# Optimization experiments

Measured on AMD Instinct MI355X. Metric: run time of the kernel, lower is better.

The kernel has to match this reference:

```python
import jax, jax.numpy as jnp
import numpy as np
from jax import lax

NL = 2        # num mamba layers
D_MODEL = 200
D_STATE = 16
D_CONV = 4
DI = 400      # expand * d_model
DT_RANK = 13  # ceil(d_model / 16)
B = 256
L = 256
EPS = 1e-12


def _ln(x, w, b):
    mu = jnp.mean(x, axis=-1, keepdims=True)
    var = jnp.mean((x - mu) ** 2, axis=-1, keepdims=True)
    return (x - mu) / jnp.sqrt(var + EPS) * w + b


def _mamba(x, in_proj_w, conv_w, conv_b, x_proj_w, dt_proj_w, dt_proj_b, A_log, D, out_proj_w):
    b, l, _ = x.shape
    xz = jnp.einsum('bld,ed->ble', x, in_proj_w)  # [b,l,2*DI]
    xc, z = jnp.split(xz, 2, axis=-1)
    # causal depthwise conv over time (pad d_conv-1 on the left == pytorch pad+slice)
    xt = xc.transpose(0, 2, 1)  # [b,DI,l]
    xt = lax.conv_general_dilated(xt, conv_w[:, None, :], (1,), [(D_CONV - 1, 0)],
                                  dimension_numbers=('NCH', 'OIH', 'NCH'),
                                  feature_group_count=DI)
    xc = jax.nn.silu(xt + conv_b[None, :, None]).transpose(0, 2, 1)  # [b,l,DI]
    x_dbl = jnp.einsum('bld,ed->ble', xc, x_proj_w)  # [b,l,DT_RANK+2*N]
    dt = x_dbl[..., :DT_RANK]
    Bm = x_dbl[..., DT_RANK:DT_RANK + D_STATE]
    Cm = x_dbl[..., DT_RANK + D_STATE:]
    delta = jax.nn.softplus(jnp.einsum('blr,dr->bld', dt, dt_proj_w) + dt_proj_b)  # [b,l,DI]
    A = -jnp.exp(A_log)  # [DI,N]

    def step(h, inp):
        d_t, u_t, B_t, C_t = inp  # [b,DI],[b,DI],[b,N],[b,N]
        dA = jnp.exp(d_t[..., None] * A)  # [b,DI,N]
        h = dA * h + (d_t * u_t)[..., None] * B_t[:, None, :]
        y = jnp.einsum('bdn,bn->bd', h, C_t)
        return h, y

    h0 = jnp.zeros((b, DI, D_STATE), dtype=x.dtype)
    xs = (delta.transpose(1, 0, 2), xc.transpose(1, 0, 2),
          Bm.transpose(1, 0, 2), Cm.transpose(1, 0, 2))
    _, ys = lax.scan(step, h0, xs)
    y = ys.transpose(1, 0, 2) + xc * D  # [b,l,DI]
    y = y * jax.nn.silu(z)
    return jnp.einsum('bld,ed->ble', y, out_proj_w)


def _forward(item_emb, in_proj_w, conv_w, conv_b, x_proj_w, dt_proj_w, dt_proj_b,
             A_log, D, out_proj_w, ln1_w, ln1_b, ffn_w1, ffn_b1, ffn_w2, ffn_b2,
             ffn_ln_w, ffn_ln_b):
    h = item_emb
    for i in range(NL):
        m = _mamba(h, in_proj_w[i], conv_w[i], conv_b[i], x_proj_w[i],
                   dt_proj_w[i], dt_proj_b[i], A_log[i], D[i], out_proj_w[i])
        h = _ln(m + h, ln1_w[i], ln1_b[i])  # num_layers > 1 -> residual branch
        f = jnp.einsum('bld,ed->ble', h, ffn_w1[i]) + ffn_b1[i]
        f = jax.nn.gelu(f, approximate=False)  # torch nn.GELU default = exact
        f = jnp.einsum('ble,de->bld', f, ffn_w2[i]) + ffn_b2[i]
        h = _ln(f + h, ffn_ln_w[i], ffn_ln_b[i])
    c = h[:, -1:, :]
    x_n = h[:, :-1, :]
    return c, x_n


def setup_inputs() -> dict:
    key = jax.random.key(0)
    ks = jax.random.split(key, 10)
    s = 0.02
    f32 = jnp.float32
    A_log = jnp.broadcast_to(jnp.log(jnp.arange(1, D_STATE + 1, dtype=f32)),
                             (NL, DI, D_STATE))
    return {
        'item_emb': jax.random.normal(ks[0], (B, L, D_MODEL), f32),
        'item_seq_len': jax.random.randint(ks[1], (B,), 1, L, jnp.int32),
        'in_proj_w': s * jax.random.normal(ks[2], (NL, 2 * DI, D_MODEL), f32),
        'conv_w': s * jax.random.normal(ks[3], (NL, DI, D_CONV), f32),
        'conv_b': jnp.zeros((NL, DI), f32),
        'x_proj_w': s * jax.random.normal(ks[4], (NL, DT_RANK + 2 * D_STATE, DI), f32),
        'dt_proj_w': s * jax.random.normal(ks[5], (NL, DI, DT_RANK), f32),
        'dt_proj_b': s * jax.random.normal(ks[6], (NL, DI), f32),
        'A_log': A_log,
        'D': jnp.ones((NL, DI), f32),
        'out_proj_w': s * jax.random.normal(ks[7], (NL, D_MODEL, DI), f32),
        'ln1_w': jnp.ones((NL, D_MODEL), f32),
        'ln1_b': jnp.zeros((NL, D_MODEL), f32),
        'ffn_w1': s * jax.random.normal(ks[8], (NL, 4 * D_MODEL, D_MODEL), f32),
        'ffn_b1': jnp.zeros((NL, 4 * D_MODEL), f32),
        'ffn_w2': s * jax.random.normal(ks[9], (NL, D_MODEL, 4 * D_MODEL), f32),
        'ffn_b2': jnp.zeros((NL, D_MODEL), f32),
        'ffn_ln_w': jnp.ones((NL, D_MODEL), f32),
        'ffn_ln_b': jnp.zeros((NL, D_MODEL), f32),
    }


def reference(item_emb, item_seq_len, in_proj_w, conv_w, conv_b, x_proj_w,
              dt_proj_w, dt_proj_b, A_log, D, out_proj_w, ln1_w, ln1_b,
              ffn_w1, ffn_b1, ffn_w2, ffn_b2, ffn_ln_w, ffn_ln_b):
    # item_seq_len is accepted but unused by Mamba4Rec.forward
    return _forward(item_emb, in_proj_w, conv_w, conv_b, x_proj_w, dt_proj_w,
                    dt_proj_b, A_log, D, out_proj_w, ln1_w, ln1_b, ffn_w1,
                    ffn_b1, ffn_w2, ffn_b2, ffn_ln_w, ffn_ln_b)
```

## Files before the change

### kernel.cpp

```cpp
#include <hip/hip_runtime.h>
#include <hip/hip_bf16.h>

#define DM 200
#define DIE 400
#define LSEQ 256
#define NB 256

typedef __hip_bfloat16 bf16;
typedef const float* fp;
typedef __attribute__((ext_vector_type(8))) short short8;
typedef __attribute__((ext_vector_type(4))) short short4_t;
typedef __attribute__((ext_vector_type(4))) float f32x4;

__device__ __forceinline__ float b2f(bf16 x) { return __bfloat162float(x); }
__device__ __forceinline__ bf16  f2b(float x) { return __float2bfloat16(x); }

__device__ __forceinline__ unsigned short f2bbits(float f) {
    union { float f; unsigned int u; } c; c.f = f;
    unsigned int u = c.u;
    unsigned int r = (u + 0x7fffu + ((u >> 16) & 1u)) >> 16;
    return (unsigned short)r;
}
__device__ __forceinline__ void stf(float* p, float v) { *p = v; }
__device__ __forceinline__ void stf(bf16* p, float v) { *p = f2b(v); }

#define W_XP_OFF 320000
#define W_OP_OFF 356000
#define W_F1_OFF 516000
#define W_F2_OFF 836000
#define W_TOTAL  1156000
#define W_BYTES  2312000

__global__ __launch_bounds__(256) void wcvt_kernel(fp a0, fp a1, fp a2, fp a3, fp a4,
                                                   bf16* __restrict__ dst) {
    int g = blockIdx.x * 256 + threadIdx.x;
    if (g >= W_TOTAL / 4) return;
    int idx = g * 4;
    const float* src;
    int off;
    if (idx < W_XP_OFF)      { src = a0; off = idx; }
    else if (idx < W_OP_OFF) { src = a1; off = idx - W_XP_OFF; }
    else if (idx < W_F1_OFF) { src = a2; off = idx - W_OP_OFF; }
    else if (idx < W_F2_OFF) { src = a3; off = idx - W_F1_OFF; }
    else                     { src = a4; off = idx - W_F2_OFF; }
    float4 v = *(const float4*)(src + off);
    short4_t o;
    o.x = (short)f2bbits(v.x); o.y = (short)f2bbits(v.y);
    o.z = (short)f2bbits(v.z); o.w = (short)f2bbits(v.w);
    *(short4_t*)((short*)dst + idx) = o;
}

__global__ __launch_bounds__(256) void cvt_kernel(const float* __restrict__ src,
                                                  bf16* __restrict__ dst, int n4) {
    int g = blockIdx.x * 256 + threadIdx.x;
    if (g >= n4) return;
    int idx = g * 4;
    float4 v = *(const float4*)(src + idx);
    short4_t o;
    o.x = (short)f2bbits(v.x); o.y = (short)f2bbits(v.y);
    o.z = (short)f2bbits(v.z); o.w = (short)f2bbits(v.w);
    *(short4_t*)((short*)dst + idx) = o;
}

template <typename TC, int EPI>
__global__ __launch_bounds__(256) void gemm_mfma(const bf16* __restrict__ A, int lda,
                                                 const bf16* __restrict__ W,
                                                 const float* __restrict__ bias,
                                                 TC* __restrict__ C, int ldc,
                                                 int N, int K) {
    constexpr int LS = 40;
    __shared__ short As[128 * LS];
    __shared__ short Bs[128 * LS];
    const int m0 = blockIdx.x * 128;
    const int n0 = blockIdx.y * 128;
    const int tid = threadIdx.x;
    const int wave = tid >> 6;
    const int lane = tid & 63;
    const int wm = (wave & 1) * 64;
    const int wn = (wave >> 1) * 64;
    const int fm = lane & 15;
    const int quad = lane >> 4;

    f32x4 acc[4][4] = {};

    const int sr = tid >> 1;
    const int sc = (tid & 1) * 16;

    for (int k0 = 0; k0 < K; k0 += 32) {
        {
            const short* src = (const short*)A + (size_t)(m0 + sr) * lda + k0 + sc;
            short* dst = As + sr * LS + sc;
            if (k0 + sc + 16 <= K) {
                *(short8*)dst = *(const short8*)src;
                *(short8*)(dst + 8) = *(const short8*)(src + 8);
            } else {
#pragma unroll
                for (int j = 0; j < 16; ++j)
                    dst[j] = (k0 + sc + j < K) ? src[j] : (short)0;
            }
        }
        {
            short* dst = Bs + sr * LS + sc;
            if (n0 + sr < N) {
                const short* src = (const short*)W + (size_t)(n0 + sr) * K + k0 + sc;
                if (k0 + sc + 16 <= K) {
                    *(short8*)dst = *(const short8*)src;
                    *(short8*)(dst + 8) = *(const short8*)(src + 8);
                } else {
#pragma unroll
                    for (int j = 0; j < 16; ++j)
                        dst[j] = (k0 + sc + j < K) ? src[j] : (short)0;
                }
            } else {
#pragma unroll
                for (int j = 0; j < 16; ++j) dst[j] = 0;
            }
        }
        __syncthreads();
        short8 af[4], bfr[4];
#pragma unroll
        for (int i = 0; i < 4; ++i)
            af[i] = *(const short8*)(As + (wm + i * 16 + fm) * LS + quad * 8);
#pragma unroll
        for (int j = 0; j < 4; ++j)
            bfr[j] = *(const short8*)(Bs + (wn + j * 16 + fm) * LS + quad * 8);
#pragma unroll
        for (int i = 0; i < 4; ++i)
#pragma unroll
            for (int j = 0; j < 4; ++j)
                acc[i][j] = __builtin_amdgcn_mfma_f32_16x16x32_bf16(af[i], bfr[j], acc[i][j], 0, 0, 0);
        __syncthreads();
    }

#pragma unroll
    for (int j = 0; j < 4; ++j) {
        int n = n0 + wn + j * 16 + fm;
        if (n >= N) continue;
        float bv = (EPI == 2 || EPI == 3) ? bias[n] : 0.f;
#pragma unroll
        for (int i = 0; i < 4; ++i) {
#pragma unroll
            for (int r = 0; r < 4; ++r) {
                int m = m0 + wm + i * 16 + quad * 4 + r;
                float v = acc[i][j][r];
                if (EPI == 2) {
                    v += bv;
                    v = 0.5f * v * (1.f + erff(v * 0.70710678118654752f));
                } else if (EPI == 3) {
                    v += bv;
                } else if (EPI == 5) {
                    if (n >= 400) v = v * __builtin_amdgcn_rcpf(1.f + __expf(-v));
                }
                stf(&C[(size_t)m * ldc + n], v);
            }
        }
    }
}

__global__ __launch_bounds__(256) void conv_silu_inplace(bf16* __restrict__ xz,
                                                         const float* __restrict__ cw,
                                                         const float* __restrict__ cb,
                                                         int total ) {
    int idx = blockIdx.x * 256 + threadIdx.x;
    if (idx >= total) return;
    int d = idx % DIE;
    int b = idx / DIE;
    float w0 = cw[d * 4 + 0];
    float w1 = cw[d * 4 + 1];
    float w2 = cw[d * 4 + 2];
    float w3 = cw[d * 4 + 3];
    float bias = cb[d];
    float x0 = 0.f, x1 = 0.f, x2 = 0.f;
    bf16* p = xz + (size_t)b * LSEQ * 800 + d;
    for (int t = 0; t < LSEQ; ++t) {
        float x = b2f(*p);
        float s = bias + w0 * x0 + w1 * x1 + w2 * x2 + w3 * x;
        x0 = x1; x1 = x2; x2 = x;
        float sig = __builtin_amdgcn_rcpf(1.f + __expf(-s));
        *p = f2b(s * sig);
        p += 800;
    }
}

template <bool FAST>
__device__ __forceinline__ void scan_body(const float* __restrict__ rp,
                                          bf16* __restrict__ xp,
                                          const float* Wr, const float* A2,
                                          float bdt, float Dv) {
    float h[16];
#pragma unroll
    for (int n = 0; n < 16; ++n) h[n] = 0.f;

    auto precomp = [&](int o45, int ox,
                       float* Bb, float* Cb, float* dA, float& du, float& ut, float& zs) {
        float dtv = bdt;
#pragma unroll
        for (int r = 0; r < 13; ++r) dtv += Wr[r] * rp[o45 + r];
#pragma unroll
        for (int j = 0; j < 16; ++j) { Bb[j] = rp[o45 + 13 + j]; Cb[j] = rp[o45 + 29 + j]; }
        ut = b2f(xp[ox]);
        zs = b2f(xp[ox + 400]);
        float sp = (dtv > 20.f) ? dtv : __logf(1.f + __expf(dtv));
        if (FAST) {
            float r1 = __expf(-sp);
            float r2 = r1 * r1, r3 = r2 * r1, r4 = r2 * r2;
            float r5 = r4 * r1, r6 = r4 * r2, r7 = r4 * r3, r8 = r4 * r4;
            dA[0] = r1;  dA[1] = r2;  dA[2] = r3;  dA[3] = r4;
            dA[4] = r5;  dA[5] = r6;  dA[6] = r7;  dA[7] = r8;
            dA[8] = r8 * r1;  dA[9] = r8 * r2;  dA[10] = r8 * r3;  dA[11] = r8 * r4;
            dA[12] = r8 * r5; dA[13] = r8 * r6; dA[14] = r8 * r7;  dA[15] = r8 * r8;
        } else {
#pragma unroll
            for (int n = 0; n < 16; ++n) dA[n] = __expf(sp * A2[n]);
        }
        du = sp * ut;
    };
    auto compute = [&](const float* Bb, const float* Cb, const float* dA,
                       float du, float ut, float zs, int ox) {
#pragma unroll
        for (int n = 0; n < 16; ++n) h[n] = dA[n] * h[n] + du * Bb[n];
        float y0 = 0.f, y1 = 0.f, y2 = 0.f, y3 = 0.f;
#pragma unroll
        for (int n = 0; n < 4; ++n) {
            y0 += h[n] * Cb[n];
            y1 += h[4 + n] * Cb[4 + n];
            y2 += h[8 + n] * Cb[8 + n];
            y3 += h[12 + n] * Cb[12 + n];
        }
        float yv = (y0 + y1) + (y2 + y3) + ut * Dv;
        xp[ox] = f2b(yv * zs);
    };

    float BA[16], CA[16], dAA[16], BB[16], CB[16], dAB[16];
    float duA, utA, zsA, duB, utB, zsB;

    precomp(0, 0, BA, CA, dAA, duA, utA, zsA);

    for (int t = 0; t < LSEQ; t += 2) {
        precomp(45, 800, BB, CB, dAB, duB, utB, zsB);
        compute(BA, CA, dAA, duA, utA, zsA, 0);
        if (t + 2 < LSEQ)
            precomp(90, 1600, BA, CA, dAA, duA, utA, zsA);
        compute(BB, CB, dAB, duB, utB, zsB, 800);
        rp += 90; xp += 1600;
    }
}

__global__ __launch_bounds__(256) void scan_kernel(const float* __restrict__ xdbl,
                                                   bf16* __restrict__ xz,
                                                   const float* __restrict__ dt_w,
                                                   const float* __restrict__ dt_b,
                                                   const float* __restrict__ A_log,
                                                   const float* __restrict__ Dw) {
    const int b = blockIdx.x >> 1;
    const int half = blockIdx.x & 1;
    const int tid = threadIdx.x;
    if (tid >= 200) return;
    const int d = half * 200 + tid;

    float A2[16], Wr[13];
    bool fast = true;
#pragma unroll
    for (int n = 0; n < 16; ++n) {
        A2[n] = -__expf(A_log[d * 16 + n]);
        fast = fast && (fabsf(A2[n] + (float)(n + 1)) < 1e-3f);
    }
#pragma unroll
    for (int r = 0; r < 13; ++r) Wr[r] = dt_w[d * 13 + r];
    const float bdt = dt_b[d];
    const float Dv = Dw[d];

    const float* __restrict__ rp = xdbl + (size_t)b * LSEQ * 45;
    bf16* __restrict__ xp = xz + (size_t)b * LSEQ * 800 + d;

    if (fast) scan_body<true>(rp, xp, Wr, A2, bdt, Dv);
    else      scan_body<false>(rp, xp, Wr, A2, bdt, Dv);
}

__global__ __launch_bounds__(256) void ln_res_kernel(const float* __restrict__ xa,
                                                     const float* xb,
                                                     const float* __restrict__ w,
                                                     const float* __restrict__ bias,
                                                     float* dst,
                                                     bf16* __restrict__ dstb, int rows,
                                                     float* __restrict__ outp, int b0) {
    int wave = threadIdx.x >> 6;
    int lane = threadIdx.x & 63;
    int row = blockIdx.x * 4 + wave;
    if (row >= rows) return;
    const float* pa = xa + (size_t)row * DM;
    const float* pb = xb + (size_t)row * DM;
    float v[4];
    float sum = 0.f, sq = 0.f;
#pragma unroll
    for (int i = 0; i < 4; ++i) {
        int c = lane + i * 64;
        float t = 0.f;
        if (c < DM) t = pa[c] + pb[c];
        v[i] = t;
        sum += t;
        sq += t * t;
    }
#pragma unroll
    for (int off = 32; off > 0; off >>= 1) {
        sum += __shfl_down(sum, off);
        sq += __shfl_down(sq, off);
    }
    sum = __shfl(sum, 0);
    sq = __shfl(sq, 0);
    float mu = sum * (1.f / DM);
    float var = fmaxf(sq * (1.f / DM) - mu * mu, 0.f);
    float rstd = rsqrtf(var + 1e-12f);
    if (outp) {
        int bb = b0 + row / LSEQ;
        int l = row % LSEQ;
        float* po = (l == LSEQ - 1)
                        ? outp + (size_t)bb * DM
                        : outp + (size_t)NB * DM + (size_t)(bb * (LSEQ - 1) + l) * DM;
#pragma unroll
        for (int i = 0; i < 4; ++i) {
            int c = lane + i * 64;
            if (c < DM) po[c] = (v[i] - mu) * rstd * w[c] + bias[c];
        }
    } else {
        float* pd = dst + (size_t)row * DM;
        bf16* pdb = dstb + (size_t)row * DM;
#pragma unroll
        for (int i = 0; i < 4; ++i) {
            int c = lane + i * 64;
            if (c < DM) {
                float o = (v[i] - mu) * rstd * w[c] + bias[c];
                pd[c] = o;
                pdb[c] = f2b(o);
            }
        }
    }
}

extern "C" void kernel_launch(void* const* d_in, const int* in_sizes, int n_in,
                              void* d_out, int out_size, void* d_ws, size_t ws_size,
                              hipStream_t stream) {
    fp emb       = (fp)d_in[0];
    fp in_proj_w = (fp)d_in[2];
    fp conv_w    = (fp)d_in[3];
    fp conv_b    = (fp)d_in[4];
    fp x_proj_w  = (fp)d_in[5];
    fp dt_proj_w = (fp)d_in[6];
    fp dt_proj_b = (fp)d_in[7];
    fp A_log     = (fp)d_in[8];
    fp Dw        = (fp)d_in[9];
    fp out_proj_w= (fp)d_in[10];
    fp ln1_w     = (fp)d_in[11];
    fp ln1_b     = (fp)d_in[12];
    fp ffn_w1    = (fp)d_in[13];
    fp ffn_b1    = (fp)d_in[14];
    fp ffn_w2    = (fp)d_in[15];
    fp ffn_b2    = (fp)d_in[16];
    fp ffn_ln_w  = (fp)d_in[17];
    fp ffn_ln_b  = (fp)d_in[18];

    const int cands[8] = {256, 128, 64, 32, 16, 8, 4, 2};
    int cb = 2;
    for (int ci = 0; ci < 8; ++ci) {
        size_t rcx = (size_t)cands[ci] * LSEQ;
        if (rcx * 3780 + W_BYTES + 1024 <= ws_size) { cb = cands[ci]; break; }
    }
    const size_t rc = (size_t)cb * LSEQ;

    bf16*  wb   = (bf16*)d_ws;
    bf16*  xz   = (bf16*)((char*)d_ws + W_BYTES);
    bf16*  hb   = xz + rc * 800;
    float* xdbl = (float*)(hb + rc * 200);
    float* m    = xdbl + rc * 45;
    float* h    = m + rc * 200;

    wcvt_kernel<<<(W_TOTAL / 4 + 255) / 256, 256, 0, stream>>>(
        in_proj_w, x_proj_w, out_proj_w, ffn_w1, ffn_w2, wb);

    const int rcDM = (int)rc * DM;
    const int gm = (int)rc / 128;

    for (int b0 = 0; b0 < NB; b0 += cb) {
        const float* emb_chunk = emb + (size_t)b0 * LSEQ * DM;

        cvt_kernel<<<(rcDM / 4 + 255) / 256, 256, 0, stream>>>(emb_chunk, hb, rcDM / 4);

        for (int i = 0; i < 2; ++i) {
            const bf16* wb_in = wb + (size_t)i * 160000;
            const bf16* wb_xp = wb + W_XP_OFF + (size_t)i * 18000;
            const bf16* wb_op = wb + W_OP_OFF + (size_t)i * 80000;
            const bf16* wb_f1 = wb + W_F1_OFF + (size_t)i * 160000;
            const bf16* wb_f2 = wb + W_F2_OFF + (size_t)i * 160000;
            fp cw    = conv_w + (size_t)i * 400 * 4;
            fp cbp   = conv_b + (size_t)i * 400;
            fp w_dt  = dt_proj_w + (size_t)i * 400 * 13;
            fp b_dt  = dt_proj_b + (size_t)i * 400;
            fp Ai    = A_log + (size_t)i * 400 * 16;
            fp Di    = Dw + (size_t)i * 400;
            fp l1w   = ln1_w + (size_t)i * 200;
            fp l1b   = ln1_b + (size_t)i * 200;
            fp f1b   = ffn_b1 + (size_t)i * 800;
            fp f2b_  = ffn_b2 + (size_t)i * 200;
            fp flw   = ffn_ln_w + (size_t)i * 200;
            fp flb   = ffn_ln_b + (size_t)i * 200;

            const float* hin = (i == 0) ? emb_chunk : h;
            const bool last = (i == 1);

            gemm_mfma<bf16, 5><<<dim3(gm, 7), 256, 0, stream>>>(
                hb, 200, wb_in, nullptr, xz, 800, 800, 200);
            conv_silu_inplace<<<(cb * DIE + 255) / 256, 256, 0, stream>>>(xz, cw, cbp, cb * DIE);
            gemm_mfma<float, 0><<<dim3(gm, 1), 256, 0, stream>>>(
                xz, 800, wb_xp, nullptr, xdbl, 45, 45, 400);
            scan_kernel<<<cb * 2, 256, 0, stream>>>(xdbl, xz, w_dt, b_dt, Ai, Di);
            gemm_mfma<float, 0><<<dim3(gm, 2), 256, 0, stream>>>(
                xz, 800, wb_op, nullptr, m, 200, 200, 400);
            ln_res_kernel<<<rc / 4, 256, 0, stream>>>(m, hin, l1w, l1b, h, hb, (int)rc,
                                                      nullptr, 0);
            gemm_mfma<bf16, 2><<<dim3(gm, 7), 256, 0, stream>>>(
                hb, 200, wb_f1, f1b, xz, 800, 800, 200);
            gemm_mfma<float, 3><<<dim3(gm, 2), 256, 0, stream>>>(
                xz, 800, wb_f2, f2b_, m, 200, 200, 800);
            ln_res_kernel<<<rc / 4, 256, 0, stream>>>(m, h, flw, flb, h, hb, (int)rc,
                                                      last ? (float*)d_out : nullptr, b0);
        }
    }
}
```

Measured before the change: 1.311 ms.

## Use direct global-to-LDS loads with swizzle in GEMM and batch scan input prefetch

The GEMM main loop now issues global_load_lds 16-byte transfers into an unpadded, XOR-swizzled LDS layout instead of staging through registers. The K remainder moves to a separate tail pass that zero-fills. Separately, the selective scan prefetches the u/z activations for the next 8 timesteps into registers one group ahead, to hide global load latency on the serial recurrence. The scan change raises register pressure, and the GEMM assumes the M and N row bounds are in range for the bulk loads.

```diff
diff --git a/kernel.cpp b/kernel.cpp
--- a/kernel.cpp
+++ b/kernel.cpp
@@ -23,6 +23,12 @@
 }
 __device__ __forceinline__ void stf(float* p, float v) { *p = v; }
 __device__ __forceinline__ void stf(bf16* p, float v) { *p = f2b(v); }
+
+__device__ __forceinline__ void gl_lds16(const void* g, void* l) {
+    __builtin_amdgcn_global_load_lds(
+        (const __attribute__((address_space(1))) unsigned int*)g,
+        (__attribute__((address_space(3))) unsigned int*)l, 16, 0, 0);
+}
 
 #define W_XP_OFF 320000
 #define W_OP_OFF 356000
@@ -68,9 +74,9 @@
                                                  const float* __restrict__ bias,
                                                  TC* __restrict__ C, int ldc,
                                                  int N, int K) {
-    constexpr int LS = 40;
-    __shared__ short As[128 * LS];
-    __shared__ short Bs[128 * LS];
+    constexpr int LSH = 32;
+    __shared__ short As[128 * LSH];
+    __shared__ short Bs[128 * LSH];
     const int m0 = blockIdx.x * 128;
     const int n0 = blockIdx.y * 128;
     const int tid = threadIdx.x;
@@ -83,47 +89,65 @@
 
     f32x4 acc[4][4] = {};
 
-    const int sr = tid >> 1;
-    const int sc = (tid & 1) * 16;
-
-    for (int k0 = 0; k0 < K; k0 += 32) {
-        {
-            const short* src = (const short*)A + (size_t)(m0 + sr) * lda + k0 + sc;
-            short* dst = As + sr * LS + sc;
-            if (k0 + sc + 16 <= K) {
-                *(short8*)dst = *(const short8*)src;
-                *(short8*)(dst + 8) = *(const short8*)(src + 8);
-            } else {
-#pragma unroll
-                for (int j = 0; j < 16; ++j)
-                    dst[j] = (k0 + sc + j < K) ? src[j] : (short)0;
-            }
-        }
-        {
-            short* dst = Bs + sr * LS + sc;
-            if (n0 + sr < N) {
-                const short* src = (const short*)W + (size_t)(n0 + sr) * K + k0 + sc;
-                if (k0 + sc + 16 <= K) {
-                    *(short8*)dst = *(const short8*)src;
-                    *(short8*)(dst + 8) = *(const short8*)(src + 8);
-                } else {
-#pragma unroll
-                    for (int j = 0; j < 16; ++j)
-                        dst[j] = (k0 + sc + j < K) ? src[j] : (short)0;
-                }
-            } else {
-#pragma unroll
-                for (int j = 0; j < 16; ++j) dst[j] = 0;
-            }
+    const int srow = tid >> 2;
+    const int o16s = (tid & 3) ^ ((tid >> 3) & 3);
+    const int ldsoff = (tid >> 6) * 1024;
+
+    const int rsl = (quad ^ ((fm >> 1) & 3)) * 8;
+
+    const int kfull = K & ~31;
+
+    for (int k0 = 0; k0 < kfull; k0 += 32) {
+#pragma unroll
+        for (int r = 0; r < 2; ++r) {
+            const short* ga = (const short*)A + (size_t)(m0 + r * 64 + srow) * lda + k0 + o16s * 8;
+            gl_lds16(ga, (char*)As + r * 4096 + ldsoff);
+            const short* gb = (const short*)W + (size_t)(n0 + r * 64 + srow) * K + k0 + o16s * 8;
+            gl_lds16(gb, (char*)Bs + r * 4096 + ldsoff);
         }
         __syncthreads();
         short8 af[4], bfr[4];
 #pragma unroll
         for (int i = 0; i < 4; ++i)
-            af[i] = *(const short8*)(As + (wm + i * 16 + fm) * LS + quad * 8);
+            af[i] = *(const short8*)(As + (wm + i * 16 + fm) * LSH + rsl);
 #pragma unroll
         for (int j = 0; j < 4; ++j)
-            bfr[j] = *(const short8*)(Bs + (wn + j * 16 + fm) * LS + quad * 8);
+            bfr[j] = *(const short8*)(Bs + (wn + j * 16 + fm) * LSH + rsl);
+#pragma unroll
+        for (int i = 0; i < 4; ++i)
+#pragma unroll
+            for (int j = 0; j < 4; ++j)
+                acc[i][j] = __builtin_amdgcn_mfma_f32_16x16x32_bf16(af[i], bfr[j], acc[i][j], 0, 0, 0);
+        __syncthreads();
+    }
+
+    if (K & 31) {
+        const int trow = tid >> 1;
+        const int tswz = (trow >> 1) & 3;
+#pragma unroll
+        for (int sl = 0; sl < 2; ++sl) {
+            const int slot = (tid & 1) * 2 + sl;
+            short ta[8], tb[8];
+            const short* sa = (const short*)A + (size_t)(m0 + trow) * lda + kfull + slot * 8;
+            const short* sb = (const short*)W + (size_t)(n0 + trow) * K + kfull + slot * 8;
+            const bool brow = (n0 + trow < N);
+#pragma unroll
+            for (int e = 0; e < 8; ++e) {
+                const bool kok = (kfull + slot * 8 + e < K);
+                ta[e] = kok ? sa[e] : (short)0;
+                tb[e] = (kok && brow) ? sb[e] : (short)0;
+            }
+            *(short8*)(As + trow * LSH + (slot ^ tswz) * 8) = *(const short8*)ta;
+            *(short8*)(Bs + trow * LSH + (slot ^ tswz) * 8) = *(const short8*)tb;
+        }
+        __syncthreads();
+        short8 af[4], bfr[4];
+#pragma unroll
+        for (int i = 0; i < 4; ++i)
+            af[i] = *(const short8*)(As + (wm + i * 16 + fm) * LSH + rsl);
+#pragma unroll
+        for (int j = 0; j < 4; ++j)
+            bfr[j] = *(const short8*)(Bs + (wn + j * 16 + fm) * LSH + rsl);
 #pragma unroll
         for (int i = 0; i < 4; ++i)
 #pragma unroll
@@ -191,15 +215,17 @@
 #pragma unroll
     for (int n = 0; n < 16; ++n) h[n] = 0.f;
 
-    auto precomp = [&](int o45, int ox,
+    float BA[16], CA[16], dAA[16], duA, utA, zsA;
+    float BB[16], CB[16], dAB[16], duB, utB, zsB;
+
+    auto precomp = [&](int o45, float utv, float zvv,
                        float* Bb, float* Cb, float* dA, float& du, float& ut, float& zs) {
         float dtv = bdt;
 #pragma unroll
         for (int r = 0; r < 13; ++r) dtv += Wr[r] * rp[o45 + r];
 #pragma unroll
         for (int j = 0; j < 16; ++j) { Bb[j] = rp[o45 + 13 + j]; Cb[j] = rp[o45 + 29 + j]; }
-        ut = b2f(xp[ox]);
-        zs = b2f(xp[ox + 400]);
+        ut = utv; zs = zvv;
         float sp = (dtv > 20.f) ? dtv : __logf(1.f + __expf(dtv));
         if (FAST) {
             float r1 = __expf(-sp);
@@ -231,18 +257,39 @@
         xp[ox] = f2b(yv * zs);
     };
 
-    float BA[16], CA[16], dAA[16], BB[16], CB[16], dAB[16];
-    float duA, utA, zsA, duB, utB, zsB;
-
-    precomp(0, 0, BA, CA, dAA, duA, utA, zsA);
-
-    for (int t = 0; t < LSEQ; t += 2) {
-        precomp(45, 800, BB, CB, dAB, duB, utB, zsB);
-        compute(BA, CA, dAA, duA, utA, zsA, 0);
-        if (t + 2 < LSEQ)
-            precomp(90, 1600, BA, CA, dAA, duA, utA, zsA);
-        compute(BB, CB, dAB, duB, utB, zsB, 800);
-        rp += 90; xp += 1600;
+    float cu[8], cz[8], nu[8], nz[8];
+#pragma unroll
+    for (int j = 0; j < 8; ++j) {
+        cu[j] = b2f(xp[j * 800]);
+        cz[j] = b2f(xp[j * 800 + 400]);
+    }
+
+    precomp(0, cu[0], cz[0], BA, CA, dAA, duA, utA, zsA);
+
+    for (int g = 0; g < LSEQ / 8; ++g) {
+        const bool more = (g + 1 < LSEQ / 8);
+        if (more) {
+#pragma unroll
+            for (int j = 0; j < 8; ++j) {
+                nu[j] = b2f(xp[(8 + j) * 800]);
+                nz[j] = b2f(xp[(8 + j) * 800 + 400]);
+            }
+        }
+#pragma unroll
+        for (int jj = 0; jj < 4; ++jj) {
+            const int j0 = 2 * jj, j1 = 2 * jj + 1;
+            precomp(j1 * 45, cu[j1], cz[j1], BB, CB, dAB, duB, utB, zsB);
+            compute(BA, CA, dAA, duA, utA, zsA, j0 * 800);
+            if (jj < 3)
+                precomp((j1 + 1) * 45, cu[j1 + 1], cz[j1 + 1], BA, CA, dAA, duA, utA, zsA);
+            else if (more)
+                precomp(8 * 45, nu[0], nz[0], BA, CA, dAA, duA, utA, zsA);
+            compute(BB, CB, dAB, duB, utB, zsB, j1 * 800);
+        }
+#pragma unroll
+        for (int j = 0; j < 8; ++j) { cu[j] = nu[j]; cz[j] = nz[j]; }
+        rp += 8 * 45;
+        xp += 8 * 800;
     }
 }
 
```

New measurement: 1.370 ms. 4.5% more time.
